# Optimization experiments

Hardware: AMD Instinct MI355X
Metric: run time of the kernel (lower is better)

Reference implementation:

```python
import jax, jax.numpy as jnp
import numpy as np

N = 40000      # option nodes
E = 320000     # edges per edge type (avg in-degree 8)
NT = 3         # edge types
L = 3          # message-passing layers
D = 128        # node_dim
HID = 256      # hidden_dim
H = 4          # attention heads
C = HID // H   # per-head channels


def _ln(x, g, b):
    m = x.mean(-1, keepdims=True)
    v = ((x - m) ** 2).mean(-1, keepdims=True)
    return g * (x - m) * jax.lax.rsqrt(v + 1e-5) + b


def _gelu(x):
    return jax.nn.gelu(x, approximate=False)  # torch default = exact erf GELU


def _gat(h, src, dst, W, a_src, a_dst, bias):
    # PyG GATConv: shared src/dst linear, add_self_loops=False, eval (no dropout)
    xp = (h @ W).reshape(N, H, C)                      # (N,H,C)
    e = jax.nn.leaky_relu((xp * a_src).sum(-1)[src] + (xp * a_dst).sum(-1)[dst], 0.2)  # (E,H)
    emax = jax.ops.segment_max(e, dst, num_segments=N)
    emax = jnp.where(jnp.isfinite(emax), emax, 0.0)    # nodes with no in-edges
    ex = jnp.exp(e - emax[dst])
    den = jax.ops.segment_sum(ex, dst, num_segments=N)
    alpha = ex / (den[dst] + 1e-16)                    # segment softmax over incoming edges
    out = jax.ops.segment_sum(alpha[:, :, None] * xp[src], dst, num_segments=N)
    return out.reshape(N, HID) + bias


def _glorot(key, shape):
    fan_in = shape[-2] if len(shape) > 1 else shape[-1]
    return jax.random.normal(key, shape, jnp.float32) / np.sqrt(fan_in)


def setup_inputs() -> dict:
    key = jax.random.key(0)
    ks = jax.random.split(key, 16)
    return {
        "x": jax.random.normal(ks[0], (N, D), jnp.float32),
        "liquidity_features": jax.random.normal(ks[1], (N, 4), jnp.float32),
        "edge_index": jax.random.randint(ks[2], (NT, 2, E), 0, N, jnp.int32),
        "edge_weight": jax.random.uniform(ks[3], (NT, E), jnp.float32),
        "in_W": _glorot(ks[4], (D, HID)), "in_b": jnp.zeros((HID,)),
        "in_g": jnp.ones((HID,)), "in_bb": jnp.zeros((HID,)),
        "gat_W": _glorot(ks[5], (L, NT, HID, HID)),
        "gat_asrc": _glorot(ks[6], (L, NT, H, C)) * 0.1,
        "gat_adst": _glorot(ks[7], (L, NT, H, C)) * 0.1,
        "gat_bias": jnp.zeros((L, NT, HID)),
        "ln_g": jnp.ones((L, HID)), "ln_b": jnp.zeros((L, HID)),
        "gate_W": _glorot(ks[8], (HID + 4, 1)), "gate_b": jnp.zeros((1,)),
        "out_W1": _glorot(ks[9], (HID, HID)), "out_b1": jnp.zeros((HID,)),
        "out_g": jnp.ones((HID,)), "out_bb": jnp.zeros((HID,)),
        "out_W2": _glorot(ks[10], (HID, D)), "out_b2": jnp.zeros((D,)),
        "ro_W1": _glorot(ks[11], (D, HID)), "ro_b1": jnp.zeros((HID,)),
        "ro_W2": _glorot(ks[12], (HID, HID)), "ro_b2": jnp.zeros((HID,)),
    }


def reference(x, liquidity_features, edge_index, edge_weight, in_W, in_b, in_g, in_bb,
              gat_W, gat_asrc, gat_adst, gat_bias, ln_g, ln_b, gate_W, gate_b,
              out_W1, out_b1, out_g, out_bb, out_W2, out_b2,
              ro_W1, ro_b1, ro_W2, ro_b2):
    h = _gelu(_ln(x @ in_W + in_b, in_g, in_bb))  # input_proj
    # incoming edge-weight gate (static graph -> identical every layer)
    wsum = jnp.zeros((N,), x.dtype)
    deg = jnp.zeros((N,), x.dtype)
    for t in range(NT):
        dst = edge_index[t, 1]
        wsum = wsum.at[dst].add(edge_weight[t])
        deg = deg.at[dst].add(1.0)
    ewg = (0.5 + jax.nn.sigmoid(wsum / jnp.maximum(deg, 1.0)))[:, None]  # (N,1)
    layer_outputs = []
    for i in range(L):
        agg = jnp.zeros((N, HID), x.dtype)  # HeteroConv aggr='sum'
        for t in range(NT):
            agg = agg + _gat(h, edge_index[t, 0], edge_index[t, 1],
                             gat_W[i, t], gat_asrc[i, t], gat_adst[i, t], gat_bias[i, t])
        gate = jax.nn.sigmoid(jnp.concatenate([agg, liquidity_features], -1) @ gate_W + gate_b)
        hn = (gate * agg + (1.0 - gate) * h) * ewg   # liquidity gate + edge-weight gate
        h = _gelu(_ln(hn + h, ln_g[i], ln_b[i]))     # residual + LayerNorm + GELU
        layer_outputs.append(h)
    ho = _gelu(_ln(h @ out_W1 + out_b1, out_g, out_bb)) @ out_W2 + out_b2  # (N,D)
    surf = _gelu(ho.mean(0) @ ro_W1 + ro_b1) @ ro_W2 + ro_b2               # (HID,)
    return (ho, surf, *layer_outputs)
```

## Files before the change

### kernel.cpp

```cpp
#include <hip/hip_runtime.h>
#include <hip/hip_bf16.h>
#include <math.h>

#define NN 40000
#define EE 320000
#define NT 3
#define LL 3
#define DD 128
#define HID 256
#define NH 4
#define CC 64
#define NP 768
#define LGRID 2048

typedef __attribute__((ext_vector_type(8))) short short8;
typedef __attribute__((ext_vector_type(4))) float f32x4;

__device__ __forceinline__ float gelu_f(float x) {
    return 0.5f * x * (1.0f + erff(x * 0.70710678118654752440f));
}
__device__ __forceinline__ float lrelu_f(float x) {
    return x > 0.0f ? x : 0.2f * x;
}
__device__ __forceinline__ float bf2f(unsigned short u) {
    unsigned int x = ((unsigned int)u) << 16;
    float f;
    __builtin_memcpy(&f, &x, 4);
    return f;
}
__device__ __forceinline__ unsigned short f2bf(float f) {
    __hip_bfloat16 h = __float2bfloat16(f);
    unsigned short u;
    __builtin_memcpy(&u, &h, 2);
    return u;
}
__device__ __forceinline__ void gload16(const void* g, void* l) {
    __builtin_amdgcn_global_load_lds(
        (const __attribute__((address_space(1))) unsigned int*)g,
        (__attribute__((address_space(3))) unsigned int*)l, 16, 0, 0);
}

__global__ void wconv_k(const float* __restrict__ W, unsigned short* __restrict__ Wt,
                        int nmat, int K, int N) {
    int idx = blockIdx.x * 256 + threadIdx.x;
    int tot = nmat * K * N;
    if (idx >= tot) return;
    int m = idx / (K * N);
    int rem = idx - m * (K * N);
    int k = rem / N;
    int n = rem - k * N;
    Wt[(size_t)m * K * N + (size_t)n * K + k] = f2bf(W[idx]);
}

__global__ void xconv_k(const float* __restrict__ x, unsigned short* __restrict__ xb) {
    int idx = blockIdx.x * 256 + threadIdx.x;
    if (idx >= NN * DD / 4) return;
    float4 v = *reinterpret_cast<const float4*>(&x[(size_t)idx * 4]);
    ushort4 o;
    o.x = f2bf(v.x); o.y = f2bf(v.y); o.z = f2bf(v.z); o.w = f2bf(v.w);
    *reinterpret_cast<ushort4*>(&xb[(size_t)idx * 4]) = o;
}

__global__ __launch_bounds__(256) void gemm_mfma_k(const unsigned short* __restrict__ A,
                                                   const unsigned short* __restrict__ Bt,
                                                   const float* __restrict__ bias,
                                                   float* __restrict__ Cf,
                                                   unsigned short* __restrict__ Cb,
                                                   int M, int K, int N) {
    __shared__ __align__(16) short As[128 * 32];
    __shared__ __align__(16) short Bs[128 * 32];
    int gdx = gridDim.x;
    int nwg = gdx * gridDim.y;
    int f = blockIdx.y * gdx + blockIdx.x;
    int q8 = nwg >> 3, r8 = nwg & 7;
    int xcd = f & 7, idx8 = f >> 3;
    int nf = (xcd < r8 ? xcd * (q8 + 1) : r8 * (q8 + 1) + (xcd - r8) * q8) + idx8;
    int bn = (nf % gdx) * 128;
    int bm = (nf / gdx) * 128;
    int tid = threadIdx.x;
    int lane = tid & 63, w = tid >> 6;
    int wr = w >> 1, wc = w & 1;
    int l16 = lane & 15, kgrp = lane >> 4;
    f32x4 acc[4][4] = {};
    for (int k0 = 0; k0 < K; k0 += 32) {
        #pragma unroll
        for (int i = 0; i < 2; i++) {
            int chunk = (i * 4 + w) * 64 + lane;
            int row = chunk >> 2, kq = chunk & 3;
            int grow = bm + row; if (grow > M - 1) grow = M - 1;
            gload16(A + (size_t)grow * K + k0 + kq * 8, &As[(i * 4 + w) * 512]);
        }
        #pragma unroll
        for (int i = 0; i < 2; i++) {
            int chunk = (i * 4 + w) * 64 + lane;
            int row = chunk >> 2, kq = chunk & 3;
            gload16(Bt + (size_t)(bn + row) * K + k0 + kq * 8, &Bs[(i * 4 + w) * 512]);
        }
        __syncthreads();
        short8 af[4], bf[4];
        #pragma unroll
        for (int mi = 0; mi < 4; mi++) {
            int row = wr * 64 + mi * 16 + l16;
            af[mi] = *reinterpret_cast<const short8*>(&As[row * 32 + kgrp * 8]);
        }
        #pragma unroll
        for (int ni = 0; ni < 4; ni++) {
            int nrow = wc * 64 + ni * 16 + l16;
            bf[ni] = *reinterpret_cast<const short8*>(&Bs[nrow * 32 + kgrp * 8]);
        }
        #pragma unroll
        for (int mi = 0; mi < 4; mi++)
            #pragma unroll
            for (int ni = 0; ni < 4; ni++)
                acc[mi][ni] = __builtin_amdgcn_mfma_f32_16x16x32_bf16(af[mi], bf[ni], acc[mi][ni], 0, 0, 0);
        __syncthreads();
    }
    #pragma unroll
    for (int mi = 0; mi < 4; mi++) {
        #pragma unroll
        for (int r = 0; r < 4; r++) {
            int row = bm + wr * 64 + mi * 16 + (lane >> 4) * 4 + r;
            if (row < M) {
                #pragma unroll
                for (int ni = 0; ni < 4; ni++) {
                    int col = bn + wc * 64 + ni * 16 + l16;
                    float v = acc[mi][ni][r] + (bias ? bias[col] : 0.0f);
                    if (Cf) Cf[(size_t)row * N + col] = v;
                    if (Cb) Cb[(size_t)row * N + col] = f2bf(v);
                }
            }
        }
    }
}

__global__ __launch_bounds__(256) void ln_gelu_k(const float* __restrict__ y,
                                                 const float* __restrict__ g,
                                                 const float* __restrict__ b,
                                                 float* __restrict__ outf,
                                                 unsigned short* __restrict__ outb) {
    int n = blockIdx.x * 4 + (threadIdx.x >> 6);
    int lane = threadIdx.x & 63;
    float4 v = *reinterpret_cast<const float4*>(&y[(size_t)n * HID + lane * 4]);
    float s = v.x + v.y + v.z + v.w;
    float q = v.x * v.x + v.y * v.y + v.z * v.z + v.w * v.w;
    #pragma unroll
    for (int o = 32; o; o >>= 1) { s += __shfl_xor(s, o); q += __shfl_xor(q, o); }
    float mean = s * (1.0f / HID);
    float var = q * (1.0f / HID) - mean * mean;
    float rs = rsqrtf(var + 1e-5f);
    float4 gv = *reinterpret_cast<const float4*>(&g[lane * 4]);
    float4 bv = *reinterpret_cast<const float4*>(&b[lane * 4]);
    float o0 = gelu_f(gv.x * (v.x - mean) * rs + bv.x);
    float o1 = gelu_f(gv.y * (v.y - mean) * rs + bv.y);
    float o2 = gelu_f(gv.z * (v.z - mean) * rs + bv.z);
    float o3 = gelu_f(gv.w * (v.w - mean) * rs + bv.w);
    if (outf) {
        float4 ov = {o0, o1, o2, o3};
        *reinterpret_cast<float4*>(&outf[(size_t)n * HID + lane * 4]) = ov;
    }
    ushort4 ob;
    ob.x = f2bf(o0); ob.y = f2bf(o1); ob.z = f2bf(o2); ob.w = f2bf(o3);
    *reinterpret_cast<ushort4*>(&outb[(size_t)n * HID + lane * 4]) = ob;
}

__global__ void hist_k(const int* __restrict__ ei, int* __restrict__ cnt) {
    int gid = blockIdx.x * 256 + threadIdx.x;
    if (gid >= NT * EE) return;
    int t = gid / EE, e = gid - t * EE;
    int dst = ei[(size_t)t * 2 * EE + EE + e];
    atomicAdd(&cnt[t * NN + dst], 1);
}

__global__ __launch_bounds__(256) void scan1_k(const int* __restrict__ cnt, int* __restrict__ bsum, int n) {
    int i = blockIdx.x * 256 + threadIdx.x;
    int v = (i < n) ? cnt[i] : 0;
    #pragma unroll
    for (int o = 32; o; o >>= 1) v += __shfl_xor(v, o);
    __shared__ int s4[4];
    if ((threadIdx.x & 63) == 0) s4[threadIdx.x >> 6] = v;
    __syncthreads();
    if (threadIdx.x == 0) bsum[blockIdx.x] = s4[0] + s4[1] + s4[2] + s4[3];
}

__global__ __launch_bounds__(512) void scan2_k(const int* __restrict__ bsum, int* __restrict__ boff, int nb) {
    __shared__ int sh[512];
    int t = threadIdx.x;
    int v = (t < nb) ? bsum[t] : 0;
    sh[t] = v;
    __syncthreads();
    for (int o = 1; o < 512; o <<= 1) {
        int tv = (t >= o) ? sh[t - o] : 0;
        __syncthreads();
        sh[t] += tv;
        __syncthreads();
    }
    if (t < nb) boff[t] = sh[t] - v;
}

__global__ __launch_bounds__(256) void scan3_k(const int* __restrict__ cnt, const int* __restrict__ boff,
                                               int* __restrict__ roff, int n) {
    int i = blockIdx.x * 256 + threadIdx.x;
    int lane = threadIdx.x & 63, w = threadIdx.x >> 6;
    int v = (i < n) ? cnt[i] : 0;
    int s = v;
    #pragma unroll
    for (int o = 1; o < 64; o <<= 1) {
        int tv = __shfl_up(s, o);
        if (lane >= o) s += tv;
    }
    __shared__ int ws_[4];
    if (lane == 63) ws_[w] = s;
    __syncthreads();
    int add = 0;
    for (int k = 0; k < 4; k++) if (k < w) add += ws_[k];
    int incl = s + add + boff[blockIdx.x];
    if (i < n) roff[i] = incl - v;
    if (i == n - 1) roff[n] = incl;
}

__global__ void scatter_k(const int* __restrict__ ei, const float* __restrict__ ew,
                          const int* __restrict__ roff, int* __restrict__ cur,
                          int* __restrict__ csr_src, float* __restrict__ csr_ew) {
    int gid = blockIdx.x * 256 + threadIdx.x;
    if (gid >= NT * EE) return;
    int t = gid / EE, e = gid - t * EE;
    int src = ei[(size_t)t * 2 * EE + e];
    int dst = ei[(size_t)t * 2 * EE + EE + e];
    int pos = roff[t * NN + dst] + atomicAdd(&cur[t * NN + dst], 1);
    csr_src[pos] = src;
    csr_ew[pos] = ew[gid];
}

__global__ void ewg_kernel(const int* __restrict__ roff, const float* __restrict__ csr_ew,
                           float* __restrict__ ewg) {
    int n = blockIdx.x * 256 + threadIdx.x;
    if (n >= NN) return;
    float ws = 0.0f;
    int dg = 0;
    for (int t = 0; t < NT; t++) {
        int beg = roff[t * NN + n], end = roff[t * NN + n + 1];
        dg += end - beg;
        for (int e = beg; e < end; e++) ws += csr_ew[e];
    }
    float m = dg > 1 ? (float)dg : 1.0f;
    float z = ws / m;
    ewg[n] = 0.5f + 1.0f / (1.0f + __expf(-z));
}

__global__ __launch_bounds__(256) void compute_s_k(const unsigned short* __restrict__ xpa,
                                                   const float* __restrict__ asrc,
                                                   const float* __restrict__ adst,
                                                   float* __restrict__ ss,
                                                   float* __restrict__ sd) {
    int t = blockIdx.x / (NN / 4);
    int node = (blockIdx.x % (NN / 4)) * 4 + (threadIdx.x >> 6);
    int lane = threadIdx.x & 63;
    ushort4 v = *reinterpret_cast<const ushort4*>(&xpa[(size_t)node * NP + t * HID + lane * 4]);
    float4 av = *reinterpret_cast<const float4*>(&asrc[t * HID + lane * 4]);
    float4 dv = *reinterpret_cast<const float4*>(&adst[t * HID + lane * 4]);
    float x0 = bf2f(v.x), x1 = bf2f(v.y), x2 = bf2f(v.z), x3 = bf2f(v.w);
    float p = x0 * av.x + x1 * av.y + x2 * av.z + x3 * av.w;
    float q = x0 * dv.x + x1 * dv.y + x2 * dv.z + x3 * dv.w;
    #pragma unroll
    for (int o = 8; o; o >>= 1) { p += __shfl_xor(p, o); q += __shfl_xor(q, o); }
    if ((lane & 15) == 0) {
        ss[((size_t)t * NN + node) * NH + (lane >> 4)] = p;
        sd[((size_t)t * NN + node) * NH + (lane >> 4)] = q;
    }
}

__global__ __launch_bounds__(256) void layer_k(const unsigned short* __restrict__ xpa,
                                               const float* __restrict__ ss,
                                               const float* __restrict__ sd,
                                               const int* __restrict__ roff,
                                               const int* __restrict__ rsrc,
                                               const float* __restrict__ gatb,
                                               const float* __restrict__ liq,
                                               const float* __restrict__ gW,
                                               const float* __restrict__ gb,
                                               const float* __restrict__ ewg,
                                               const float* __restrict__ lg,
                                               const float* __restrict__ lb,
                                               float* __restrict__ hout,
                                               unsigned short* __restrict__ hb) {
    int wid = blockIdx.x * 4 + (threadIdx.x >> 6);
    int lane = threadIdx.x & 63;
    int h = lane >> 4;
    const int nw = LGRID * 4;
    float4 bb0 = *reinterpret_cast<const float4*>(&gatb[lane * 4]);
    float4 bb1 = *reinterpret_cast<const float4*>(&gatb[HID + lane * 4]);
    float4 bb2 = *reinterpret_cast<const float4*>(&gatb[2 * HID + lane * 4]);
    float bs0 = bb0.x + bb1.x + bb2.x;
    float bs1 = bb0.y + bb1.y + bb2.y;
    float bs2 = bb0.z + bb1.z + bb2.z;
    float bs3 = bb0.w + bb1.w + bb2.w;
    float4 gwv = *reinterpret_cast<const float4*>(&gW[lane * 4]);
    float gwl = (lane < 4) ? gW[HID + lane] : 0.0f;
    float gb0 = gb[0];
    float4 lgv = *reinterpret_cast<const float4*>(&lg[lane * 4]);
    float4 lbv = *reinterpret_cast<const float4*>(&lb[lane * 4]);

    for (int node = wid; node < NN; node += nw) {
        float agg0 = 0, agg1 = 0, agg2 = 0, agg3 = 0;
        #pragma unroll
        for (int t = 0; t < NT; t++) {
            int base = t * NN;
            int beg = roff[base + node], end = roff[base + node + 1];
            if (beg == end) continue;
            float sdh = sd[(size_t)(base + node) * NH + h];
            float den = 0, a0 = 0, a1 = 0, a2 = 0, a3 = 0;
            int last = end - 1;
            for (int e = beg; e < end; e += 4) {
                int e1 = e + 1 > last ? last : e + 1;
                int e2 = e + 2 > last ? last : e + 2;
                int e3 = e + 3 > last ? last : e + 3;
                int s0 = rsrc[e], s1 = rsrc[e1], s2 = rsrc[e2], s3 = rsrc[e3];
                float sv0 = ss[(size_t)(base + s0) * NH + h];
                float sv1 = ss[(size_t)(base + s1) * NH + h];
                float sv2 = ss[(size_t)(base + s2) * NH + h];
                float sv3 = ss[(size_t)(base + s3) * NH + h];
                ushort4 x0 = *reinterpret_cast<const ushort4*>(&xpa[(size_t)s0 * NP + t * HID + lane * 4]);
                ushort4 x1 = *reinterpret_cast<const ushort4*>(&xpa[(size_t)s1 * NP + t * HID + lane * 4]);
                ushort4 x2 = *reinterpret_cast<const ushort4*>(&xpa[(size_t)s2 * NP + t * HID + lane * 4]);
                ushort4 x3 = *reinterpret_cast<const ushort4*>(&xpa[(size_t)s3 * NP + t * HID + lane * 4]);
                float w0 = __expf(lrelu_f(sv0 + sdh));
                float w1 = (e + 1 <= last) ? __expf(lrelu_f(sv1 + sdh)) : 0.0f;
                float w2 = (e + 2 <= last) ? __expf(lrelu_f(sv2 + sdh)) : 0.0f;
                float w3 = (e + 3 <= last) ? __expf(lrelu_f(sv3 + sdh)) : 0.0f;
                den += (w0 + w1) + (w2 + w3);
                a0 += w0 * bf2f(x0.x) + w1 * bf2f(x1.x) + w2 * bf2f(x2.x) + w3 * bf2f(x3.x);
                a1 += w0 * bf2f(x0.y) + w1 * bf2f(x1.y) + w2 * bf2f(x2.y) + w3 * bf2f(x3.y);
                a2 += w0 * bf2f(x0.z) + w1 * bf2f(x1.z) + w2 * bf2f(x2.z) + w3 * bf2f(x3.z);
                a3 += w0 * bf2f(x0.w) + w1 * bf2f(x1.w) + w2 * bf2f(x2.w) + w3 * bf2f(x3.w);
            }
            float inv = 1.0f / (den + 1e-16f);
            agg0 += a0 * inv; agg1 += a1 * inv; agg2 += a2 * inv; agg3 += a3 * inv;
        }
        agg0 += bs0; agg1 += bs1; agg2 += bs2; agg3 += bs3;
        float part = agg0 * gwv.x + agg1 * gwv.y + agg2 * gwv.z + agg3 * gwv.w;
        if (lane < 4) part += liq[node * 4 + lane] * gwl;
        #pragma unroll
        for (int o = 32; o; o >>= 1) part += __shfl_xor(part, o);
        float gate = 1.0f / (1.0f + __expf(-(part + gb0)));
        float eg = ewg[node];
        ushort4 hu = *reinterpret_cast<const ushort4*>(&hb[(size_t)node * HID + lane * 4]);
        float h0 = bf2f(hu.x), h1 = bf2f(hu.y), h2 = bf2f(hu.z), h3 = bf2f(hu.w);
        float v0 = (gate * agg0 + (1.0f - gate) * h0) * eg + h0;
        float v1 = (gate * agg1 + (1.0f - gate) * h1) * eg + h1;
        float v2 = (gate * agg2 + (1.0f - gate) * h2) * eg + h2;
        float v3 = (gate * agg3 + (1.0f - gate) * h3) * eg + h3;
        float s = v0 + v1 + v2 + v3;
        float q = v0 * v0 + v1 * v1 + v2 * v2 + v3 * v3;
        #pragma unroll
        for (int o = 32; o; o >>= 1) { s += __shfl_xor(s, o); q += __shfl_xor(q, o); }
        float mean = s * (1.0f / HID);
        float var = q * (1.0f / HID) - mean * mean;
        float rs = rsqrtf(var + 1e-5f);
        float o0 = gelu_f(lgv.x * (v0 - mean) * rs + lbv.x);
        float o1 = gelu_f(lgv.y * (v1 - mean) * rs + lbv.y);
        float o2 = gelu_f(lgv.z * (v2 - mean) * rs + lbv.z);
        float o3 = gelu_f(lgv.w * (v3 - mean) * rs + lbv.w);
        float4 ov = {o0, o1, o2, o3};
        *reinterpret_cast<float4*>(&hout[(size_t)node * HID + lane * 4]) = ov;
        ushort4 ob;
        ob.x = f2bf(o0); ob.y = f2bf(o1); ob.z = f2bf(o2); ob.w = f2bf(o3);
        *reinterpret_cast<ushort4*>(&hb[(size_t)node * HID + lane * 4]) = ob;
    }
}

__global__ __launch_bounds__(128) void colpart_k(const float* __restrict__ ho,
                                                 float* __restrict__ part) {
    int c = threadIdx.x, b = blockIdx.x;
    float s = 0.0f;
    for (int r = b; r < NN; r += 256) s += ho[(size_t)r * DD + c];
    part[b * DD + c] = s;
}

__global__ __launch_bounds__(256) void readout_k(const float* __restrict__ part,
                                                 const float* __restrict__ W1,
                                                 const float* __restrict__ b1,
                                                 const float* __restrict__ W2,
                                                 const float* __restrict__ b2,
                                                 float* __restrict__ surf) {
    __shared__ float m[DD];
    __shared__ float a1[HID];
    int t = threadIdx.x;
    if (t < DD) {
        float s = 0.0f;
        for (int b = 0; b < 256; b++) s += part[b * DD + t];
        m[t] = s / (float)NN;
    }
    __syncthreads();
    float s1 = b1[t];
    for (int k = 0; k < DD; k++) s1 += m[k] * W1[k * HID + t];
    a1[t] = gelu_f(s1);
    __syncthreads();
    float s2 = b2[t];
    for (int k = 0; k < HID; k++) s2 += a1[k] * W2[k * HID + t];
    surf[t] = s2;
}

extern "C" void kernel_launch(void* const* d_in, const int* in_sizes, int n_in,
                              void* d_out, int out_size, void* d_ws, size_t ws_size,
                              hipStream_t stream) {
    const float* x       = (const float*)d_in[0];
    const float* liq     = (const float*)d_in[1];
    const int*   ei      = (const int*)d_in[2];
    const float* ew      = (const float*)d_in[3];
    const float* in_W    = (const float*)d_in[4];
    const float* in_b    = (const float*)d_in[5];
    const float* in_g    = (const float*)d_in[6];
    const float* in_bb   = (const float*)d_in[7];
    const float* gat_W   = (const float*)d_in[8];
    const float* gat_as  = (const float*)d_in[9];
    const float* gat_ad  = (const float*)d_in[10];
    const float* gat_b   = (const float*)d_in[11];
    const float* ln_g    = (const float*)d_in[12];
    const float* ln_b    = (const float*)d_in[13];
    const float* gate_W  = (const float*)d_in[14];
    const float* gate_b  = (const float*)d_in[15];
    const float* out_W1  = (const float*)d_in[16];
    const float* out_b1  = (const float*)d_in[17];
    const float* out_g   = (const float*)d_in[18];
    const float* out_bb  = (const float*)d_in[19];
    const float* out_W2  = (const float*)d_in[20];
    const float* out_b2  = (const float*)d_in[21];
    const float* ro_W1   = (const float*)d_in[22];
    const float* ro_b1   = (const float*)d_in[23];
    const float* ro_W2   = (const float*)d_in[24];
    const float* ro_b2   = (const float*)d_in[25];

    float* out = (float*)d_out;
    float* out_ho   = out;
    float* out_surf = out + (size_t)NN * DD;
    float* out_h[3];
    out_h[0] = out_surf + HID;
    out_h[1] = out_h[0] + (size_t)NN * HID;
    out_h[2] = out_h[1] + (size_t)NN * HID;

    char* wsb = (char*)d_ws;
    size_t off = 0;
    auto alloc = [&](size_t bytes) { char* p = wsb + off; off += (bytes + 255) & ~(size_t)255; return p; };
    unsigned short* xpa = (unsigned short*)alloc((size_t)NN * NP * 2);
    float* Cf32 = (float*)xpa;
    unsigned short* xb = xpa + (size_t)NN * 512;
    unsigned short* hb = (unsigned short*)alloc((size_t)NN * HID * 2);
    unsigned short* Wt_in  = (unsigned short*)alloc((size_t)DD * HID * 2);
    unsigned short* Wt_gat = (unsigned short*)alloc((size_t)LL * NT * HID * HID * 2);
    unsigned short* Wt_o1  = (unsigned short*)alloc((size_t)HID * HID * 2);
    unsigned short* Wt_o2  = (unsigned short*)alloc((size_t)HID * DD * 2);
    size_t cew_b = (size_t)NT * EE * 4;
    size_t cnt_b = (size_t)NT * NN * 4;
    char* R = alloc(cew_b + cnt_b + 2 * 2048 * 4);
    float* cew = (float*)R;
    int* cnt   = (int*)(R + cew_b);
    int* bsum  = (int*)(R + cew_b + cnt_b);
    int* boff  = bsum + 2048;
    float* ss  = (float*)R;
    float* sd  = ss + (size_t)NT * NN * NH;
    int* roff  = (int*)alloc(((size_t)NT * NN + 1) * 4);
    int* rsrc  = (int*)alloc((size_t)NT * EE * 4);
    float* ewg = (float*)alloc((size_t)NN * 4);
    float* cpart = (float*)alloc((size_t)256 * DD * 4);

    const int NSC = (NT * NN + 255) / 256;

    wconv_k<<<(DD * HID + 255) / 256, 256, 0, stream>>>(in_W, Wt_in, 1, DD, HID);
    wconv_k<<<(LL * NT * HID * HID + 255) / 256, 256, 0, stream>>>(gat_W, Wt_gat, LL * NT, HID, HID);
    wconv_k<<<(HID * HID + 255) / 256, 256, 0, stream>>>(out_W1, Wt_o1, 1, HID, HID);
    wconv_k<<<(HID * DD + 255) / 256, 256, 0, stream>>>(out_W2, Wt_o2, 1, HID, DD);
    xconv_k<<<(NN * DD / 4 + 255) / 256, 256, 0, stream>>>(x, xb);

    gemm_mfma_k<<<dim3(HID / 128, (NN + 127) / 128), 256, 0, stream>>>(
        xb, Wt_in, in_b, Cf32, nullptr, NN, DD, HID);
    ln_gelu_k<<<NN / 4, 256, 0, stream>>>(Cf32, in_g, in_bb, nullptr, hb);

    hipMemsetAsync(cnt, 0, cnt_b, stream);
    hist_k<<<(NT * EE + 255) / 256, 256, 0, stream>>>(ei, cnt);
    scan1_k<<<NSC, 256, 0, stream>>>(cnt, bsum, NT * NN);
    scan2_k<<<1, 512, 0, stream>>>(bsum, boff, NSC);
    scan3_k<<<NSC, 256, 0, stream>>>(cnt, boff, roff, NT * NN);
    hipMemsetAsync(cnt, 0, cnt_b, stream);
    scatter_k<<<(NT * EE + 255) / 256, 256, 0, stream>>>(ei, ew, roff, cnt, rsrc, cew);
    ewg_kernel<<<(NN + 255) / 256, 256, 0, stream>>>(roff, cew, ewg);

    for (int i = 0; i < LL; i++) {
        gemm_mfma_k<<<dim3(NP / 128, (NN + 127) / 128), 256, 0, stream>>>(
            hb, Wt_gat + (size_t)i * NP * HID, nullptr, nullptr, xpa, NN, HID, NP);
        compute_s_k<<<NT * (NN / 4), 256, 0, stream>>>(
            xpa, gat_as + (size_t)i * NT * HID, gat_ad + (size_t)i * NT * HID, ss, sd);
        layer_k<<<LGRID, 256, 0, stream>>>(
            xpa, ss, sd, roff, rsrc, gat_b + (size_t)i * NT * HID,
            liq, gate_W, gate_b, ewg, ln_g + i * HID, ln_b + i * HID,
            out_h[i], hb);
    }

    gemm_mfma_k<<<dim3(HID / 128, (NN + 127) / 128), 256, 0, stream>>>(
        hb, Wt_o1, out_b1, Cf32, nullptr, NN, HID, HID);
    ln_gelu_k<<<NN / 4, 256, 0, stream>>>(Cf32, out_g, out_bb, nullptr, hb);
    gemm_mfma_k<<<dim3(DD / 128, (NN + 127) / 128), 256, 0, stream>>>(
        hb, Wt_o2, out_b2, out_ho, nullptr, NN, HID, DD);

    colpart_k<<<256, 128, 0, stream>>>(out_ho, cpart);
    readout_k<<<1, 256, 0, stream>>>(cpart, ro_W1, ro_b1, ro_W2, ro_b2, out_surf);
}
```

Before: 814.3 us.

## Precompute W·a attention vectors and compute scores from h directly

```diff
diff --git a/kernel.cpp b/kernel.cpp
--- a/kernel.cpp
+++ b/kernel.cpp
@@ -59,6 +59,67 @@
     ushort4 o;
     o.x = f2bf(v.x); o.y = f2bf(v.y); o.z = f2bf(v.z); o.w = f2bf(v.w);
     *reinterpret_cast<ushort4*>(&xb[(size_t)idx * 4]) = o;
+}
+
+__global__ __launch_bounds__(256) void gemv_u_k(const float* __restrict__ gat_W,
+                                                const float* __restrict__ gat_as,
+                                                const float* __restrict__ gat_ad,
+                                                float* __restrict__ u) {
+    int b = blockIdx.x;
+    int k = threadIdx.x;
+    int l = b / 24;
+    int r = b - l * 24;
+    int t = r >> 3;
+    int r2 = r & 7;
+    int h = r2 >> 1;
+    int sdx = r2 & 1;
+    __shared__ float av[CC];
+    const float* a = (sdx == 0 ? gat_as : gat_ad) + (size_t)((l * NT + t) * NH + h) * CC;
+    if (k < CC) av[k] = a[k];
+    __syncthreads();
+    const float* Wrow = gat_W + ((size_t)(l * NT + t) * HID + k) * HID + h * CC;
+    float s = 0.0f;
+    #pragma unroll 8
+    for (int j = 0; j < CC; j++) s += Wrow[j] * av[j];
+    u[(size_t)b * HID + k] = s * 1.4426950408889634f;
+}
+
+__global__ __launch_bounds__(256) void score_k(const unsigned short* __restrict__ hb,
+                                               const float* __restrict__ ul,
+                                               float* __restrict__ ss,
+                                               float* __restrict__ sd) {
+    int node = blockIdx.x * 4 + (threadIdx.x >> 6);
+    int lane = threadIdx.x & 63;
+    int h = lane >> 4, m = lane & 15;
+    float xv[16];
+    #pragma unroll
+    for (int q = 0; q < 4; q++) {
+        ushort4 v = *reinterpret_cast<const ushort4*>(&hb[(size_t)node * HID + m * 16 + q * 4]);
+        xv[q * 4 + 0] = bf2f(v.x);
+        xv[q * 4 + 1] = bf2f(v.y);
+        xv[q * 4 + 2] = bf2f(v.z);
+        xv[q * 4 + 3] = bf2f(v.w);
+    }
+    #pragma unroll
+    for (int t = 0; t < NT; t++) {
+        #pragma unroll
+        for (int sdx = 0; sdx < 2; sdx++) {
+            const float* up = ul + (size_t)(((t * NH + h) * 2 + sdx)) * HID + m * 16;
+            float acc = 0.0f;
+            #pragma unroll
+            for (int q = 0; q < 4; q++) {
+                float4 uv = *reinterpret_cast<const float4*>(&up[q * 4]);
+                acc += xv[q * 4 + 0] * uv.x + xv[q * 4 + 1] * uv.y
+                     + xv[q * 4 + 2] * uv.z + xv[q * 4 + 3] * uv.w;
+            }
+            #pragma unroll
+            for (int o = 8; o; o >>= 1) acc += __shfl_xor(acc, o);
+            if (m == 0) {
+                float* dst = (sdx == 0 ? ss : sd);
+                dst[((size_t)t * NN + node) * NH + h] = acc;
+            }
+        }
+    }
 }
 
 __global__ __launch_bounds__(256) void gemm_mfma_k(const unsigned short* __restrict__ A,
@@ -247,28 +308,6 @@
     ewg[n] = 0.5f + 1.0f / (1.0f + __expf(-z));
 }
 
-__global__ __launch_bounds__(256) void compute_s_k(const unsigned short* __restrict__ xpa,
-                                                   const float* __restrict__ asrc,
-                                                   const float* __restrict__ adst,
-                                                   float* __restrict__ ss,
-                                                   float* __restrict__ sd) {
-    int t = blockIdx.x / (NN / 4);
-    int node = (blockIdx.x % (NN / 4)) * 4 + (threadIdx.x >> 6);
-    int lane = threadIdx.x & 63;
-    ushort4 v = *reinterpret_cast<const ushort4*>(&xpa[(size_t)node * NP + t * HID + lane * 4]);
-    float4 av = *reinterpret_cast<const float4*>(&asrc[t * HID + lane * 4]);
-    float4 dv = *reinterpret_cast<const float4*>(&adst[t * HID + lane * 4]);
-    float x0 = bf2f(v.x), x1 = bf2f(v.y), x2 = bf2f(v.z), x3 = bf2f(v.w);
-    float p = x0 * av.x + x1 * av.y + x2 * av.z + x3 * av.w;
-    float q = x0 * dv.x + x1 * dv.y + x2 * dv.z + x3 * dv.w;
-    #pragma unroll
-    for (int o = 8; o; o >>= 1) { p += __shfl_xor(p, o); q += __shfl_xor(q, o); }
-    if ((lane & 15) == 0) {
-        ss[((size_t)t * NN + node) * NH + (lane >> 4)] = p;
-        sd[((size_t)t * NN + node) * NH + (lane >> 4)] = q;
-    }
-}
-
 __global__ __launch_bounds__(256) void layer_k(const unsigned short* __restrict__ xpa,
                                                const float* __restrict__ ss,
                                                const float* __restrict__ sd,
@@ -287,6 +326,8 @@
     int lane = threadIdx.x & 63;
     int h = lane >> 4;
     const int nw = LGRID * 4;
+    const char* xpa_b = (const char*)xpa;
+    const char* ss_b = (const char*)ss;
     float4 bb0 = *reinterpret_cast<const float4*>(&gatb[lane * 4]);
     float4 bb1 = *reinterpret_cast<const float4*>(&gatb[HID + lane * 4]);
     float4 bb2 = *reinterpret_cast<const float4*>(&gatb[2 * HID + lane * 4]);
@@ -308,25 +349,30 @@
             int beg = roff[base + node], end = roff[base + node + 1];
             if (beg == end) continue;
             float sdh = sd[(size_t)(base + node) * NH + h];
+            unsigned int cxp = (unsigned int)(t * 512 + lane * 8);
+            unsigned int css = (unsigned int)(t * NN * 16 + h * 4);
             float den = 0, a0 = 0, a1 = 0, a2 = 0, a3 = 0;
             int last = end - 1;
             for (int e = beg; e < end; e += 4) {
                 int e1 = e + 1 > last ? last : e + 1;
                 int e2 = e + 2 > last ? last : e + 2;
                 int e3 = e + 3 > last ? last : e + 3;
-                int s0 = rsrc[e], s1 = rsrc[e1], s2 = rsrc[e2], s3 = rsrc[e3];
-                float sv0 = ss[(size_t)(base + s0) * NH + h];
-                float sv1 = ss[(size_t)(base + s1) * NH + h];
-                float sv2 = ss[(size_t)(base + s2) * NH + h];
-                float sv3 = ss[(size_t)(base + s3) * NH + h];
-                ushort4 x0 = *reinterpret_cast<const ushort4*>(&xpa[(size_t)s0 * NP + t * HID + lane * 4]);
-                ushort4 x1 = *reinterpret_cast<const ushort4*>(&xpa[(size_t)s1 * NP + t * HID + lane * 4]);
-                ushort4 x2 = *reinterpret_cast<const ushort4*>(&xpa[(size_t)s2 * NP + t * HID + lane * 4]);
-                ushort4 x3 = *reinterpret_cast<const ushort4*>(&xpa[(size_t)s3 * NP + t * HID + lane * 4]);
-                float w0 = __expf(lrelu_f(sv0 + sdh));
-                float w1 = (e + 1 <= last) ? __expf(lrelu_f(sv1 + sdh)) : 0.0f;
-                float w2 = (e + 2 <= last) ? __expf(lrelu_f(sv2 + sdh)) : 0.0f;
-                float w3 = (e + 3 <= last) ? __expf(lrelu_f(sv3 + sdh)) : 0.0f;
+                unsigned int s0 = (unsigned int)rsrc[e];
+                unsigned int s1 = (unsigned int)rsrc[e1];
+                unsigned int s2 = (unsigned int)rsrc[e2];
+                unsigned int s3 = (unsigned int)rsrc[e3];
+                float sv0 = *(const float*)(ss_b + (s0 * 16u + css));
+                float sv1 = *(const float*)(ss_b + (s1 * 16u + css));
+                float sv2 = *(const float*)(ss_b + (s2 * 16u + css));
+                float sv3 = *(const float*)(ss_b + (s3 * 16u + css));
+                ushort4 x0 = *(const ushort4*)(xpa_b + (s0 * 1536u + cxp));
+                ushort4 x1 = *(const ushort4*)(xpa_b + (s1 * 1536u + cxp));
+                ushort4 x2 = *(const ushort4*)(xpa_b + (s2 * 1536u + cxp));
+                ushort4 x3 = *(const ushort4*)(xpa_b + (s3 * 1536u + cxp));
+                float w0 = exp2f(lrelu_f(sv0 + sdh));
+                float w1 = (e + 1 <= last) ? exp2f(lrelu_f(sv1 + sdh)) : 0.0f;
+                float w2 = (e + 2 <= last) ? exp2f(lrelu_f(sv2 + sdh)) : 0.0f;
+                float w3 = (e + 3 <= last) ? exp2f(lrelu_f(sv3 + sdh)) : 0.0f;
                 den += (w0 + w1) + (w2 + w3);
                 a0 += w0 * bf2f(x0.x) + w1 * bf2f(x1.x) + w2 * bf2f(x2.x) + w3 * bf2f(x3.x);
                 a1 += w0 * bf2f(x0.y) + w1 * bf2f(x1.y) + w2 * bf2f(x2.y) + w3 * bf2f(x3.y);
@@ -462,6 +508,7 @@
     int* rsrc  = (int*)alloc((size_t)NT * EE * 4);
     float* ewg = (float*)alloc((size_t)NN * 4);
     float* cpart = (float*)alloc((size_t)256 * DD * 4);
+    float* uvec  = (float*)alloc((size_t)LL * 24 * HID * 4);
 
     const int NSC = (NT * NN + 255) / 256;
 
@@ -469,6 +516,7 @@
     wconv_k<<<(LL * NT * HID * HID + 255) / 256, 256, 0, stream>>>(gat_W, Wt_gat, LL * NT, HID, HID);
     wconv_k<<<(HID * HID + 255) / 256, 256, 0, stream>>>(out_W1, Wt_o1, 1, HID, HID);
     wconv_k<<<(HID * DD + 255) / 256, 256, 0, stream>>>(out_W2, Wt_o2, 1, HID, DD);
+    gemv_u_k<<<LL * 24, 256, 0, stream>>>(gat_W, gat_as, gat_ad, uvec);
     xconv_k<<<(NN * DD / 4 + 255) / 256, 256, 0, stream>>>(x, xb);
 
     gemm_mfma_k<<<dim3(HID / 128, (NN + 127) / 128), 256, 0, stream>>>(
@@ -487,8 +535,7 @@
     for (int i = 0; i < LL; i++) {
         gemm_mfma_k<<<dim3(NP / 128, (NN + 127) / 128), 256, 0, stream>>>(
             hb, Wt_gat + (size_t)i * NP * HID, nullptr, nullptr, xpa, NN, HID, NP);
-        compute_s_k<<<NT * (NN / 4), 256, 0, stream>>>(
-            xpa, gat_as + (size_t)i * NT * HID, gat_ad + (size_t)i * NT * HID, ss, sd);
+        score_k<<<NN / 4, 256, 0, stream>>>(hb, uvec + (size_t)i * 24 * HID, ss, sd);
         layer_k<<<LGRID, 256, 0, stream>>>(
             xpa, ss, sd, roff, rsrc, gat_b + (size_t)i * NT * HID,
             liq, gate_W, gate_b, ewg, ln_g + i * HID, ln_b + i * HID,
```

Measured after the change: 922.2 us. 1.13x slower.

## Precompute per-edge attention weights in a separate kernel before aggregation

Applied to the files above, without the earlier changes.

```diff
diff --git a/kernel.cpp b/kernel.cpp
--- a/kernel.cpp
+++ b/kernel.cpp
@@ -11,6 +11,7 @@
 #define NH 4
 #define CC 64
 #define NP 768
+#define ETOT (NT * EE)
 #define LGRID 2048
 
 typedef __attribute__((ext_vector_type(8))) short short8;
@@ -269,9 +270,38 @@
     }
 }
 
+__global__ __launch_bounds__(256) void escore_k(const float* __restrict__ ss,
+                                                const float* __restrict__ sd,
+                                                const int* __restrict__ roff,
+                                                const int* __restrict__ rsrc,
+                                                unsigned short* __restrict__ esc) {
+    int wid = blockIdx.x * 4 + (threadIdx.x >> 6);
+    int lane = threadIdx.x & 63;
+    int eo = lane >> 2;
+    int h = lane & 3;
+    const int nw = LGRID * 4;
+    for (int node = wid; node < NN; node += nw) {
+        #pragma unroll
+        for (int t = 0; t < NT; t++) {
+            int base = t * NN;
+            int beg = roff[base + node], end = roff[base + node + 1];
+            if (beg == end) continue;
+            float sdh = sd[(size_t)(base + node) * NH + h];
+            for (int e0 = beg; e0 < end; e0 += 16) {
+                int e = e0 + eo;
+                if (e < end) {
+                    int src = rsrc[e];
+                    float s = ss[(size_t)(base + src) * NH + h];
+                    float w = exp2f(lrelu_f((s + sdh) * 1.4426950408889634f));
+                    esc[(size_t)h * ETOT + e] = f2bf(w);
+                }
+            }
+        }
+    }
+}
+
 __global__ __launch_bounds__(256) void layer_k(const unsigned short* __restrict__ xpa,
-                                               const float* __restrict__ ss,
-                                               const float* __restrict__ sd,
+                                               const unsigned short* __restrict__ esc,
                                                const int* __restrict__ roff,
                                                const int* __restrict__ rsrc,
                                                const float* __restrict__ gatb,
@@ -285,8 +315,9 @@
                                                unsigned short* __restrict__ hb) {
     int wid = blockIdx.x * 4 + (threadIdx.x >> 6);
     int lane = threadIdx.x & 63;
-    int h = lane >> 4;
     const int nw = LGRID * 4;
+    const char* xpa_b = (const char*)xpa;
+    const unsigned short* wpl = esc + (size_t)(lane >> 4) * ETOT;
     float4 bb0 = *reinterpret_cast<const float4*>(&gatb[lane * 4]);
     float4 bb1 = *reinterpret_cast<const float4*>(&gatb[HID + lane * 4]);
     float4 bb2 = *reinterpret_cast<const float4*>(&gatb[2 * HID + lane * 4]);
@@ -307,26 +338,25 @@
             int base = t * NN;
             int beg = roff[base + node], end = roff[base + node + 1];
             if (beg == end) continue;
-            float sdh = sd[(size_t)(base + node) * NH + h];
+            unsigned int cxp = (unsigned int)(t * 512 + lane * 8);
             float den = 0, a0 = 0, a1 = 0, a2 = 0, a3 = 0;
             int last = end - 1;
             for (int e = beg; e < end; e += 4) {
                 int e1 = e + 1 > last ? last : e + 1;
                 int e2 = e + 2 > last ? last : e + 2;
                 int e3 = e + 3 > last ? last : e + 3;
-                int s0 = rsrc[e], s1 = rsrc[e1], s2 = rsrc[e2], s3 = rsrc[e3];
-                float sv0 = ss[(size_t)(base + s0) * NH + h];
-                float sv1 = ss[(size_t)(base + s1) * NH + h];
-                float sv2 = ss[(size_t)(base + s2) * NH + h];
-                float sv3 = ss[(size_t)(base + s3) * NH + h];
-                ushort4 x0 = *reinterpret_cast<const ushort4*>(&xpa[(size_t)s0 * NP + t * HID + lane * 4]);
-                ushort4 x1 = *reinterpret_cast<const ushort4*>(&xpa[(size_t)s1 * NP + t * HID + lane * 4]);
-                ushort4 x2 = *reinterpret_cast<const ushort4*>(&xpa[(size_t)s2 * NP + t * HID + lane * 4]);
-                ushort4 x3 = *reinterpret_cast<const ushort4*>(&xpa[(size_t)s3 * NP + t * HID + lane * 4]);
-                float w0 = __expf(lrelu_f(sv0 + sdh));
-                float w1 = (e + 1 <= last) ? __expf(lrelu_f(sv1 + sdh)) : 0.0f;
-                float w2 = (e + 2 <= last) ? __expf(lrelu_f(sv2 + sdh)) : 0.0f;
-                float w3 = (e + 3 <= last) ? __expf(lrelu_f(sv3 + sdh)) : 0.0f;
+                unsigned int s0 = (unsigned int)rsrc[e];
+                unsigned int s1 = (unsigned int)rsrc[e1];
+                unsigned int s2 = (unsigned int)rsrc[e2];
+                unsigned int s3 = (unsigned int)rsrc[e3];
+                float w0 = bf2f(wpl[e]);
+                float w1 = (e + 1 <= last) ? bf2f(wpl[e1]) : 0.0f;
+                float w2 = (e + 2 <= last) ? bf2f(wpl[e2]) : 0.0f;
+                float w3 = (e + 3 <= last) ? bf2f(wpl[e3]) : 0.0f;
+                ushort4 x0 = *(const ushort4*)(xpa_b + (s0 * 1536u + cxp));
+                ushort4 x1 = *(const ushort4*)(xpa_b + (s1 * 1536u + cxp));
+                ushort4 x2 = *(const ushort4*)(xpa_b + (s2 * 1536u + cxp));
+                ushort4 x3 = *(const ushort4*)(xpa_b + (s3 * 1536u + cxp));
                 den += (w0 + w1) + (w2 + w3);
                 a0 += w0 * bf2f(x0.x) + w1 * bf2f(x1.x) + w2 * bf2f(x2.x) + w3 * bf2f(x3.x);
                 a1 += w0 * bf2f(x0.y) + w1 * bf2f(x1.y) + w2 * bf2f(x2.y) + w3 * bf2f(x3.y);
@@ -462,6 +492,7 @@
     int* rsrc  = (int*)alloc((size_t)NT * EE * 4);
     float* ewg = (float*)alloc((size_t)NN * 4);
     float* cpart = (float*)alloc((size_t)256 * DD * 4);
+    unsigned short* esc = (unsigned short*)alloc((size_t)NH * ETOT * 2 + 64);
 
     const int NSC = (NT * NN + 255) / 256;
 
@@ -489,8 +520,9 @@
             hb, Wt_gat + (size_t)i * NP * HID, nullptr, nullptr, xpa, NN, HID, NP);
         compute_s_k<<<NT * (NN / 4), 256, 0, stream>>>(
             xpa, gat_as + (size_t)i * NT * HID, gat_ad + (size_t)i * NT * HID, ss, sd);
+        escore_k<<<LGRID, 256, 0, stream>>>(ss, sd, roff, rsrc, esc);
         layer_k<<<LGRID, 256, 0, stream>>>(
-            xpa, ss, sd, roff, rsrc, gat_b + (size_t)i * NT * HID,
+            xpa, esc, roff, rsrc, gat_b + (size_t)i * NT * HID,
             liq, gate_W, gate_b, ewg, ln_g + i * HID, ln_b + i * HID,
             out_h[i], hb);
     }
```

After: 908.4 us. 11.6% more time.
